# Optimization experiments

Measured on AMD Instinct MI355X. Metric: run time of the kernel, lower is better.

Reference implementation:

```python
import jax, jax.numpy as jnp
import numpy as np

MAX_LEN = 1024

def _lin(x, W, b=None):
    y = x @ W.T
    return y if b is None else y + b

def setup_inputs() -> dict:
    key = jax.random.key(0)
    ks = jax.random.split(key, 16)
    s = 0.05
    inp = {
        "x": jax.random.normal(ks[0], (8, 1024, 16), jnp.float32),
        "WQ": jax.random.normal(ks[1], (64, 16), jnp.float32) * s,
        "WK": jax.random.normal(ks[2], (64, 16), jnp.float32) * s,
        "VW1": jax.random.normal(ks[3], (16, 16), jnp.float32) * s,
        "Vb1": jnp.zeros((16,), jnp.float32),
        "VW2": jax.random.normal(ks[4], (16, 16), jnp.float32) * s,
        "Vb2": jnp.zeros((16,), jnp.float32),
        "VW3": jax.random.normal(ks[5], (8, 16), jnp.float32) * s,
        "Vb3": jnp.zeros((8,), jnp.float32),
        "PW1": jax.random.normal(ks[6], (64, 1), jnp.float32) * s,
        "Pb1": jnp.zeros((64,), jnp.float32),
        "PW2": jax.random.normal(ks[7], (64, 64), jnp.float32) * s,
        "Pb2": jnp.zeros((64,), jnp.float32),
        "PW3": jax.random.normal(ks[8], (64, 64), jnp.float32) * s,
        "Pb3": jnp.zeros((64,), jnp.float32),
        "PW4": jax.random.normal(ks[9], (32, 64), jnp.float32) * s,
        "Pb4": jnp.zeros((32,), jnp.float32),
        "offset": jnp.array([-10.0], jnp.float32),
        "HW1": jax.random.normal(ks[10], (256, 256), jnp.float32) * s,
        "Hb1": jnp.zeros((256,), jnp.float32),
        "HW2": jax.random.normal(ks[11], (256, 256), jnp.float32) * s,
        "Hb2": jnp.zeros((256,), jnp.float32),
        "HW3": jax.random.normal(ks[12], (4, 256), jnp.float32) * s,
        "Hb3": jnp.zeros((4,), jnp.float32),
    }
    return inp

def reference(x, WQ, WK, VW1, Vb1, VW2, Vb2, VW3, Vb3,
              PW1, Pb1, PW2, Pb2, PW3, Pb3, PW4, Pb4,
              offset, HW1, Hb1, HW2, Hb2, HW3, Hb3):
    B, L, _ = x.shape
    # Q/K projections and raw scores  [B, L, L]
    q = _lin(x, WQ)
    k = _lin(x, WK)
    a = jnp.einsum('bik,bjk->bij', q, k)
    d_k = q.shape[-1]
    # sigmoid attention with zeroed diagonal
    Iinf = 1.0 - jnp.eye(L, dtype=x.dtype)
    attention = jax.nn.sigmoid(a / jnp.sqrt(jnp.asarray(d_k, x.dtype)) + offset[0]) * Iinf
    # parametric set function: Phi MLP over t in [0,1]
    t = jnp.linspace(0.0, 1.0, MAX_LEN, dtype=x.dtype)[:L, None]  # [L, 1]
    h = jax.nn.relu(_lin(t, PW1, Pb1))
    h = jax.nn.relu(_lin(h, PW2, Pb2))
    h = jax.nn.relu(_lin(h, PW3, Pb3))
    SetPhi = _lin(h, PW4, Pb4)  # [L, set_dim]
    # relative-position gather: SetPhi[|i-j|] -> [L, L, set_dim]
    ar = jnp.arange(L)
    Tidx = jnp.abs(ar[:, None] - ar[None, :])
    rel = SetPhi[Tidx]
    set_values = jnp.einsum('bij,ijk->bik', attention, rel)  # [B, L, set_dim]
    # V MLP with sigmoid output  [B, L, vdim]
    v = jax.nn.relu(_lin(x, VW1, Vb1))
    v = jax.nn.relu(_lin(v, VW2, Vb2))
    v = jax.nn.sigmoid(_lin(v, VW3, Vb3))
    summarized = jnp.einsum('bij,bik->bjk', set_values, v)  # [B, set_dim, vdim]
    # head MLP + softmax (num_classes > 1)
    flat = summarized.reshape(B, -1)
    h = jax.nn.relu(_lin(flat, HW1, Hb1))
    h = jax.nn.relu(_lin(h, HW2, Hb2))
    return jax.nn.softmax(_lin(h, HW3, Hb3), axis=-1)
```

## Files before the change

kernel.cpp:

```cpp
#include <hip/hip_runtime.h>
#include <hip/hip_bf16.h>


#define LSEQ 1024
#define DK   64
#define EMB  16
#define VDIM 8

typedef __attribute__((ext_vector_type(8))) short bf16x8;
typedef __attribute__((ext_vector_type(4))) float f32x4;

__device__ __forceinline__ unsigned short f2bf(float f) {
  union { float f; unsigned u; } v; v.f = f;
  unsigned r = v.u + 0x7fffu + ((v.u >> 16) & 1u);
  return (unsigned short)(r >> 16);
}

__device__ __forceinline__ f32x4 mfma16(bf16x8 a, bf16x8 b, f32x4 c) {
  return __builtin_amdgcn_mfma_f32_16x16x32_bf16(a, b, c, 0, 0, 0);
}

__global__ __launch_bounds__(256) void prep_kernel(
    const float* __restrict__ x,  const float* __restrict__ WQ,  const float* __restrict__ WK,
    const float* __restrict__ VW1, const float* __restrict__ Vb1,
    const float* __restrict__ VW2, const float* __restrict__ Vb2,
    const float* __restrict__ VW3, const float* __restrict__ Vb3,
    const float* __restrict__ PW1, const float* __restrict__ Pb1,
    const float* __restrict__ PW2, const float* __restrict__ Pb2,
    const float* __restrict__ PW3, const float* __restrict__ Pb3,
    const float* __restrict__ PW4, const float* __restrict__ Pb4,
    unsigned short* __restrict__ qb, unsigned short* __restrict__ kb,
    unsigned short* __restrict__ phiT, float* __restrict__ vws,
    float* __restrict__ summar)
{
  __shared__ float s1[272];
  __shared__ float s2[272];
  int bid = blockIdx.x, tid = threadIdx.x;

  if (bid < 4096) {
    int g = bid * 256 + tid;
    int row = g >> 7, c = g & 127;
    const float* xr = x + row * EMB;
    const float* wr = ((c < 64) ? WQ : WK) + (c & 63) * EMB;
    float acc = 0.f;
    #pragma unroll
    for (int e = 0; e < 4; ++e) {
      f32x4 xv = *(const f32x4*)(xr + e * 4);
      f32x4 wv = *(const f32x4*)(wr + e * 4);
      acc += xv[0]*wv[0] + xv[1]*wv[1] + xv[2]*wv[2] + xv[3]*wv[3];
    }
    unsigned short* dst = (c < 64) ? qb : kb;
    dst[row * DK + (c & 63)] = f2bf(acc);

  } else if (bid < 4608) {
    int lb = bid - 4096;
    int r = tid >> 4, cc = tid & 15;
    int row = lb * 16 + r;
    const float* xr = x + row * EMB;
    float acc = Vb1[cc];
    #pragma unroll
    for (int e4 = 0; e4 < 4; ++e4) {
      f32x4 wv = *(const f32x4*)(VW1 + cc * 16 + e4 * 4);
      acc += xr[e4*4+0]*wv[0] + xr[e4*4+1]*wv[1] + xr[e4*4+2]*wv[2] + xr[e4*4+3]*wv[3];
    }
    s1[r * 17 + cc] = fmaxf(acc, 0.f);
    __syncthreads();
    acc = Vb2[cc];
    #pragma unroll
    for (int e4 = 0; e4 < 4; ++e4) {
      f32x4 wv = *(const f32x4*)(VW2 + cc * 16 + e4 * 4);
      acc += s1[r*17+e4*4+0]*wv[0] + s1[r*17+e4*4+1]*wv[1] + s1[r*17+e4*4+2]*wv[2] + s1[r*17+e4*4+3]*wv[3];
    }
    s2[r * 17 + cc] = fmaxf(acc, 0.f);
    __syncthreads();
    if (cc < 8) {
      acc = Vb3[cc];
      #pragma unroll
      for (int e4 = 0; e4 < 4; ++e4) {
        f32x4 wv = *(const f32x4*)(VW3 + cc * 16 + e4 * 4);
        acc += s2[r*17+e4*4+0]*wv[0] + s2[r*17+e4*4+1]*wv[1] + s2[r*17+e4*4+2]*wv[2] + s2[r*17+e4*4+3]*wv[3];
      }
      vws[row * VDIM + cc] = 1.f / (1.f + __expf(-acc));
    }

  } else if (bid < 4864) {
    int lb = bid - 4608;
    int r = tid >> 6, cc = tid & 63;
    int row = lb * 4 + r;
    float t = (float)row * (1.0f / 1023.0f);
    s1[r * 65 + cc] = fmaxf(PW1[cc] * t + Pb1[cc], 0.f);
    __syncthreads();
    float acc = Pb2[cc];
    #pragma unroll
    for (int e4 = 0; e4 < 16; ++e4) {
      f32x4 wv = *(const f32x4*)(PW2 + cc * 64 + e4 * 4);
      acc += s1[r*65+e4*4+0]*wv[0] + s1[r*65+e4*4+1]*wv[1] + s1[r*65+e4*4+2]*wv[2] + s1[r*65+e4*4+3]*wv[3];
    }
    s2[r * 65 + cc] = fmaxf(acc, 0.f);
    __syncthreads();
    acc = Pb3[cc];
    #pragma unroll
    for (int e4 = 0; e4 < 16; ++e4) {
      f32x4 wv = *(const f32x4*)(PW3 + cc * 64 + e4 * 4);
      acc += s2[r*65+e4*4+0]*wv[0] + s2[r*65+e4*4+1]*wv[1] + s2[r*65+e4*4+2]*wv[2] + s2[r*65+e4*4+3]*wv[3];
    }
    s1[r * 65 + cc] = fmaxf(acc, 0.f);
    __syncthreads();
    if (cc < 32) {
      acc = Pb4[cc];
      #pragma unroll
      for (int e4 = 0; e4 < 16; ++e4) {
        f32x4 wv = *(const f32x4*)(PW4 + cc * 64 + e4 * 4);
        acc += s1[r*65+e4*4+0]*wv[0] + s1[r*65+e4*4+1]*wv[1] + s1[r*65+e4*4+2]*wv[2] + s1[r*65+e4*4+3]*wv[3];
      }
      phiT[cc * LSEQ + row] = f2bf(acc);
    }

  } else {
    int idx = (bid - 4864) * 256 + tid;
    summar[idx] = 0.f;
  }
}

__global__ __launch_bounds__(512, 4) void attn_kernel(
    const unsigned short* __restrict__ qb, const unsigned short* __restrict__ kb,
    const unsigned short* __restrict__ phiT, const float* __restrict__ vws,
    const float* __restrict__ offs, float* __restrict__ summar)
{
  __shared__ float A2_s[16 * 1026];
  __shared__ float sv_w[8][16][17];
  __shared__ float v_s[16][8];

  int bid = blockIdx.x;
  int b  = bid >> 6;
  int i0 = (bid & 63) << 4;
  int tid = threadIdx.x;
  int lane = tid & 63, w = tid >> 6;
  int lr = lane & 15, lg = lane >> 4;

  for (int idx = tid; idx < 16 * 1026; idx += 512) A2_s[idx] = 0.f;
  if (tid < 128) v_s[tid >> 3][tid & 7] = vws[(b * LSEQ + i0 + (tid >> 3)) * VDIM + (tid & 7)];

  float off = offs[0];

  const unsigned short* qrow = qb + (size_t)(b * LSEQ + i0 + lr) * DK + lg * 8;
  bf16x8 afr0 = *(const bf16x8*)qrow;
  bf16x8 afr1 = *(const bf16x8*)(qrow + 32);

  const unsigned short* kbase = kb + (size_t)b * LSEQ * DK + (size_t)(w * 128 + lr) * DK + lg * 8;
  bf16x8 bk0[8], bk1[8];
  #pragma unroll
  for (int st = 0; st < 4; ++st) {
    bk0[2*st]   = *(const bf16x8*)(kbase + st * 16 * DK);
    bk0[2*st+1] = *(const bf16x8*)(kbase + st * 16 * DK + 32);
  }

  __syncthreads();

  #pragma unroll
  for (int st = 0; st < 4; ++st) {
    bk1[2*st]   = *(const bf16x8*)(kbase + (st + 4) * 16 * DK);
    bk1[2*st+1] = *(const bf16x8*)(kbase + (st + 4) * 16 * DK + 32);
  }

  #pragma unroll
  for (int st = 0; st < 4; ++st) {
    f32x4 acc = {0.f, 0.f, 0.f, 0.f};
    acc = mfma16(afr0, bk0[2*st], acc);
    acc = mfma16(afr1, bk0[2*st+1], acc);
    #pragma unroll
    for (int r2 = 0; r2 < 4; ++r2) {
      int row = 4 * lg + r2;
      int gi = i0 + row;
      int gj = w * 128 + st * 16 + lr;
      float s = (gi == gj) ? 0.f : 1.f / (1.f + __expf(-(acc[r2] * 0.125f + off)));
      int d = gi - gj; d = (d < 0) ? -d : d;
      unsafeAtomicAdd(&A2_s[row * 1026 + d], s);
    }
  }
  #pragma unroll
  for (int st = 0; st < 4; ++st) {
    f32x4 acc = {0.f, 0.f, 0.f, 0.f};
    acc = mfma16(afr0, bk1[2*st], acc);
    acc = mfma16(afr1, bk1[2*st+1], acc);
    #pragma unroll
    for (int r2 = 0; r2 < 4; ++r2) {
      int row = 4 * lg + r2;
      int gi = i0 + row;
      int gj = w * 128 + (st + 4) * 16 + lr;
      float s = (gi == gj) ? 0.f : 1.f / (1.f + __expf(-(acc[r2] * 0.125f + off)));
      int d = gi - gj; d = (d < 0) ? -d : d;
      unsafeAtomicAdd(&A2_s[row * 1026 + d], s);
    }
  }
  __syncthreads();

  {
    int ct = w & 1, kq = w >> 1;
    const unsigned short* ph = phiT + (ct * 16 + lr) * LSEQ + kq * 256 + lg * 8;
    bf16x8 pf[8];
    #pragma unroll
    for (int s = 0; s < 8; ++s) pf[s] = *(const bf16x8*)(ph + s * 32);
    const float* arow = A2_s + lr * 1026 + kq * 256 + lg * 8;
    f32x4 acc = {0.f, 0.f, 0.f, 0.f};
    #pragma unroll
    for (int s = 0; s < 8; ++s) {
      bf16x8 af;
      const float* ap = arow + s * 32;
      #pragma unroll
      for (int e = 0; e < 8; ++e) af[e] = (short)f2bf(ap[e]);
      acc = mfma16(af, pf[s], acc);
    }
    #pragma unroll
    for (int r2 = 0; r2 < 4; ++r2)
      sv_w[w][4 * lg + r2][lr] = acc[r2];
  }
  __syncthreads();

  if (tid < 256) {
    int sd = tid >> 3, kk = tid & 7;
    int ct = sd >> 4, cl = sd & 15;
    float a = 0.f;
    #pragma unroll
    for (int il = 0; il < 16; ++il) {
      float sv = sv_w[ct][il][cl] + sv_w[ct + 2][il][cl]
               + sv_w[ct + 4][il][cl] + sv_w[ct + 6][il][cl];
      a += sv * v_s[il][kk];
    }
    unsafeAtomicAdd(&summar[b * 256 + sd * 8 + kk], a);
  }
}

__global__ __launch_bounds__(1024) void head_kernel(
    const float* __restrict__ summar,
    const float* __restrict__ HW1, const float* __restrict__ Hb1,
    const float* __restrict__ HW2, const float* __restrict__ Hb2,
    const float* __restrict__ HW3, const float* __restrict__ Hb3,
    float* __restrict__ out)
{
  __shared__ float fb[256];
  __shared__ float part[4][260];
  __shared__ float lgt[4];
  int b = blockIdx.x, tid = threadIdx.x;
  int c = tid & 255, qt = tid >> 8;

  if (qt == 0) fb[c] = summar[b * 256 + c];
  __syncthreads();
  {
    const float* wr = HW1 + c * 256 + qt * 64;
    const float* xr = fb + qt * 64;
    float a = 0.f;
    #pragma unroll
    for (int e = 0; e < 16; ++e) {
      f32x4 wv = *(const f32x4*)(wr + e * 4);
      f32x4 xv = *(const f32x4*)(xr + e * 4);
      a += wv[0]*xv[0] + wv[1]*xv[1] + wv[2]*xv[2] + wv[3]*xv[3];
    }
    part[qt][c] = a;
  }
  __syncthreads();
  if (qt == 0)
    fb[c] = fmaxf(part[0][c] + part[1][c] + part[2][c] + part[3][c] + Hb1[c], 0.f);
  __syncthreads();
  {
    const float* wr = HW2 + c * 256 + qt * 64;
    const float* xr = fb + qt * 64;
    float a = 0.f;
    #pragma unroll
    for (int e = 0; e < 16; ++e) {
      f32x4 wv = *(const f32x4*)(wr + e * 4);
      f32x4 xv = *(const f32x4*)(xr + e * 4);
      a += wv[0]*xv[0] + wv[1]*xv[1] + wv[2]*xv[2] + wv[3]*xv[3];
    }
    part[qt][c] = a;
  }
  __syncthreads();
  if (qt == 0)
    fb[c] = fmaxf(part[0][c] + part[1][c] + part[2][c] + part[3][c] + Hb2[c], 0.f);
  __syncthreads();
  if (tid < 4) {
    float a = Hb3[tid];
    for (int e = 0; e < 256; ++e) a += fb[e] * HW3[tid * 256 + e];
    lgt[tid] = a;
  }
  __syncthreads();
  if (tid == 0) {
    float m = fmaxf(fmaxf(lgt[0], lgt[1]), fmaxf(lgt[2], lgt[3]));
    float e0 = __expf(lgt[0] - m), e1 = __expf(lgt[1] - m);
    float e2 = __expf(lgt[2] - m), e3 = __expf(lgt[3] - m);
    float s = e0 + e1 + e2 + e3;
    out[b * 4 + 0] = e0 / s;
    out[b * 4 + 1] = e1 / s;
    out[b * 4 + 2] = e2 / s;
    out[b * 4 + 3] = e3 / s;
  }
}

extern "C" void kernel_launch(void* const* d_in, const int* in_sizes, int n_in,
                              void* d_out, int out_size, void* d_ws, size_t ws_size,
                              hipStream_t stream)
{
  const float* x   = (const float*)d_in[0];
  const float* WQ  = (const float*)d_in[1];
  const float* WK  = (const float*)d_in[2];
  const float* VW1 = (const float*)d_in[3];
  const float* Vb1 = (const float*)d_in[4];
  const float* VW2 = (const float*)d_in[5];
  const float* Vb2 = (const float*)d_in[6];
  const float* VW3 = (const float*)d_in[7];
  const float* Vb3 = (const float*)d_in[8];
  const float* PW1 = (const float*)d_in[9];
  const float* Pb1 = (const float*)d_in[10];
  const float* PW2 = (const float*)d_in[11];
  const float* Pb2 = (const float*)d_in[12];
  const float* PW3 = (const float*)d_in[13];
  const float* Pb3 = (const float*)d_in[14];
  const float* PW4 = (const float*)d_in[15];
  const float* Pb4 = (const float*)d_in[16];
  const float* offs= (const float*)d_in[17];
  const float* HW1 = (const float*)d_in[18];
  const float* Hb1 = (const float*)d_in[19];
  const float* HW2 = (const float*)d_in[20];
  const float* Hb2 = (const float*)d_in[21];
  const float* HW3 = (const float*)d_in[22];
  const float* Hb3 = (const float*)d_in[23];

  char* ws = (char*)d_ws;
  unsigned short* qb   = (unsigned short*)(ws);
  unsigned short* kb   = (unsigned short*)(ws + (1u << 20));
  unsigned short* phiT = (unsigned short*)(ws + (2u << 20));
  float* vws    = (float*)(ws + (2u << 20) + (1u << 16));
  float* summar = (float*)(ws + (2u << 20) + (1u << 16) + (1u << 18));

  prep_kernel<<<dim3(4872), dim3(256), 0, stream>>>(
      x, WQ, WK, VW1, Vb1, VW2, Vb2, VW3, Vb3,
      PW1, Pb1, PW2, Pb2, PW3, Pb3, PW4, Pb4,
      qb, kb, phiT, vws, summar);

  attn_kernel<<<dim3(512), dim3(512), 0, stream>>>(
      qb, kb, phiT, vws, offs, summar);

  head_kernel<<<dim3(8), dim3(1024), 0, stream>>>(
      summar, HW1, Hb1, HW2, Hb2, HW3, Hb3, (float*)d_out);
}
```

Baseline: 189.0 us.

## Coarsen QK projection, hoist phi loads, and reduce V contraction with shuffles

The Q/K projection now has each thread compute 8 output channels for a row, cutting the prep grid from 4872 to 1288 blocks and reusing x loads. The attention kernel issues the phi fragment loads early so they overlap the zero-fill and score phase, and pads the shared A2 row stride. The final shared sv_w buffer, its barrier and the serial reduction are replaced by a per-wave multiply with V, cross-lane shuffle reduction and direct global atomics. The tradeoff is more global atomics per block and higher register pressure from holding the phi fragments live through the score phase.

```diff
diff --git a/kernel.cpp b/kernel.cpp
--- a/kernel.cpp
+++ b/kernel.cpp
@@ -6,6 +6,7 @@
 #define DK   64
 #define EMB  16
 #define VDIM 8
+#define A2S  1032
 
 typedef __attribute__((ext_vector_type(8))) short bf16x8;
 typedef __attribute__((ext_vector_type(4))) float f32x4;
@@ -37,23 +38,32 @@
   __shared__ float s2[272];
   int bid = blockIdx.x, tid = threadIdx.x;
 
-  if (bid < 4096) {
-    int g = bid * 256 + tid;
-    int row = g >> 7, c = g & 127;
+  if (bid < 512) {
+    int row = bid * 16 + (tid >> 4);
+    int c0 = (tid & 15) * 8;
     const float* xr = x + row * EMB;
-    const float* wr = ((c < 64) ? WQ : WK) + (c & 63) * EMB;
-    float acc = 0.f;
-    #pragma unroll
-    for (int e = 0; e < 4; ++e) {
-      f32x4 xv = *(const f32x4*)(xr + e * 4);
-      f32x4 wv = *(const f32x4*)(wr + e * 4);
-      acc += xv[0]*wv[0] + xv[1]*wv[1] + xv[2]*wv[2] + xv[3]*wv[3];
-    }
-    unsigned short* dst = (c < 64) ? qb : kb;
-    dst[row * DK + (c & 63)] = f2bf(acc);
-
-  } else if (bid < 4608) {
-    int lb = bid - 4096;
+    f32x4 xv0 = *(const f32x4*)(xr);
+    f32x4 xv1 = *(const f32x4*)(xr + 4);
+    f32x4 xv2 = *(const f32x4*)(xr + 8);
+    f32x4 xv3 = *(const f32x4*)(xr + 12);
+    #pragma unroll
+    for (int u = 0; u < 8; ++u) {
+      int c = c0 + u;
+      const float* wr = ((c < 64) ? WQ : WK) + (c & 63) * EMB;
+      f32x4 wv0 = *(const f32x4*)(wr);
+      f32x4 wv1 = *(const f32x4*)(wr + 4);
+      f32x4 wv2 = *(const f32x4*)(wr + 8);
+      f32x4 wv3 = *(const f32x4*)(wr + 12);
+      float acc = xv0[0]*wv0[0]+xv0[1]*wv0[1]+xv0[2]*wv0[2]+xv0[3]*wv0[3]
+                + xv1[0]*wv1[0]+xv1[1]*wv1[1]+xv1[2]*wv1[2]+xv1[3]*wv1[3]
+                + xv2[0]*wv2[0]+xv2[1]*wv2[1]+xv2[2]*wv2[2]+xv2[3]*wv2[3]
+                + xv3[0]*wv3[0]+xv3[1]*wv3[1]+xv3[2]*wv3[2]+xv3[3]*wv3[3];
+      unsigned short* dst = (c < 64) ? qb : kb;
+      dst[row * DK + (c & 63)] = f2bf(acc);
+    }
+
+  } else if (bid < 1024) {
+    int lb = bid - 512;
     int r = tid >> 4, cc = tid & 15;
     int row = lb * 16 + r;
     const float* xr = x + row * EMB;
@@ -83,8 +93,8 @@
       vws[row * VDIM + cc] = 1.f / (1.f + __expf(-acc));
     }
 
-  } else if (bid < 4864) {
-    int lb = bid - 4608;
+  } else if (bid < 1280) {
+    int lb = bid - 1024;
     int r = tid >> 6, cc = tid & 63;
     int row = lb * 4 + r;
     float t = (float)row * (1.0f / 1023.0f);
@@ -117,7 +127,7 @@
     }
 
   } else {
-    int idx = (bid - 4864) * 256 + tid;
+    int idx = (bid - 1280) * 256 + tid;
     summar[idx] = 0.f;
   }
 }
@@ -127,8 +137,7 @@
     const unsigned short* __restrict__ phiT, const float* __restrict__ vws,
     const float* __restrict__ offs, float* __restrict__ summar)
 {
-  __shared__ float A2_s[16 * 1026];
-  __shared__ float sv_w[8][16][17];
+  __shared__ float A2_s[16 * A2S];
   __shared__ float v_s[16][8];
 
   int bid = blockIdx.x;
@@ -138,25 +147,31 @@
   int lane = tid & 63, w = tid >> 6;
   int lr = lane & 15, lg = lane >> 4;
 
-  for (int idx = tid; idx < 16 * 1026; idx += 512) A2_s[idx] = 0.f;
-  if (tid < 128) v_s[tid >> 3][tid & 7] = vws[(b * LSEQ + i0 + (tid >> 3)) * VDIM + (tid & 7)];
-
-  float off = offs[0];
-
   const unsigned short* qrow = qb + (size_t)(b * LSEQ + i0 + lr) * DK + lg * 8;
   bf16x8 afr0 = *(const bf16x8*)qrow;
   bf16x8 afr1 = *(const bf16x8*)(qrow + 32);
 
+  int ct = w & 1, kq = w >> 1;
+  const unsigned short* ph = phiT + (ct * 16 + lr) * LSEQ + kq * 256 + lg * 8;
+  bf16x8 pf[8];
+  #pragma unroll
+  for (int s = 0; s < 8; ++s) pf[s] = *(const bf16x8*)(ph + s * 32);
+
   const unsigned short* kbase = kb + (size_t)b * LSEQ * DK + (size_t)(w * 128 + lr) * DK + lg * 8;
-  bf16x8 bk0[8], bk1[8];
+  bf16x8 bk0[8];
   #pragma unroll
   for (int st = 0; st < 4; ++st) {
     bk0[2*st]   = *(const bf16x8*)(kbase + st * 16 * DK);
     bk0[2*st+1] = *(const bf16x8*)(kbase + st * 16 * DK + 32);
   }
 
-  __syncthreads();
-
+  float off = offs[0];
+  if (tid < 128) v_s[tid >> 3][tid & 7] = vws[(b * LSEQ + i0 + (tid >> 3)) * VDIM + (tid & 7)];
+
+  for (int idx = tid; idx < 16 * A2S; idx += 512) A2_s[idx] = 0.f;
+  __syncthreads();
+
+  bf16x8 bk1[8];
   #pragma unroll
   for (int st = 0; st < 4; ++st) {
     bk1[2*st]   = *(const bf16x8*)(kbase + (st + 4) * 16 * DK);
@@ -175,7 +190,7 @@
       int gj = w * 128 + st * 16 + lr;
       float s = (gi == gj) ? 0.f : 1.f / (1.f + __expf(-(acc[r2] * 0.125f + off)));
       int d = gi - gj; d = (d < 0) ? -d : d;
-      unsafeAtomicAdd(&A2_s[row * 1026 + d], s);
+      unsafeAtomicAdd(&A2_s[row * A2S + d], s);
     }
   }
   #pragma unroll
@@ -190,19 +205,14 @@
       int gj = w * 128 + (st + 4) * 16 + lr;
       float s = (gi == gj) ? 0.f : 1.f / (1.f + __expf(-(acc[r2] * 0.125f + off)));
       int d = gi - gj; d = (d < 0) ? -d : d;
-      unsafeAtomicAdd(&A2_s[row * 1026 + d], s);
-    }
-  }
-  __syncthreads();
-
+      unsafeAtomicAdd(&A2_s[row * A2S + d], s);
+    }
+  }
+  __syncthreads();
+
+  f32x4 acc = {0.f, 0.f, 0.f, 0.f};
   {
-    int ct = w & 1, kq = w >> 1;
-    const unsigned short* ph = phiT + (ct * 16 + lr) * LSEQ + kq * 256 + lg * 8;
-    bf16x8 pf[8];
-    #pragma unroll
-    for (int s = 0; s < 8; ++s) pf[s] = *(const bf16x8*)(ph + s * 32);
-    const float* arow = A2_s + lr * 1026 + kq * 256 + lg * 8;
-    f32x4 acc = {0.f, 0.f, 0.f, 0.f};
+    const float* arow = A2_s + lr * A2S + kq * 256 + lg * 8;
     #pragma unroll
     for (int s = 0; s < 8; ++s) {
       bf16x8 af;
@@ -211,23 +221,33 @@
       for (int e = 0; e < 8; ++e) af[e] = (short)f2bf(ap[e]);
       acc = mfma16(af, pf[s], acc);
     }
-    #pragma unroll
-    for (int r2 = 0; r2 < 4; ++r2)
-      sv_w[w][4 * lg + r2][lr] = acc[r2];
-  }
-  __syncthreads();
-
-  if (tid < 256) {
-    int sd = tid >> 3, kk = tid & 7;
-    int ct = sd >> 4, cl = sd & 15;
-    float a = 0.f;
-    #pragma unroll
-    for (int il = 0; il < 16; ++il) {
-      float sv = sv_w[ct][il][cl] + sv_w[ct + 2][il][cl]
-               + sv_w[ct + 4][il][cl] + sv_w[ct + 6][il][cl];
-      a += sv * v_s[il][kk];
-    }
-    unsafeAtomicAdd(&summar[b * 256 + sd * 8 + kk], a);
+  }
+
+  {
+    float p[8];
+    #pragma unroll
+    for (int kk = 0; kk < 8; ++kk) p[kk] = 0.f;
+    #pragma unroll
+    for (int r2 = 0; r2 < 4; ++r2) {
+      int row = 4 * lg + r2;
+      f32x4 va = *(const f32x4*)&v_s[row][0];
+      f32x4 vb = *(const f32x4*)&v_s[row][4];
+      p[0] += acc[r2] * va[0];  p[1] += acc[r2] * va[1];
+      p[2] += acc[r2] * va[2];  p[3] += acc[r2] * va[3];
+      p[4] += acc[r2] * vb[0];  p[5] += acc[r2] * vb[1];
+      p[6] += acc[r2] * vb[2];  p[7] += acc[r2] * vb[3];
+    }
+    #pragma unroll
+    for (int kk = 0; kk < 8; ++kk) {
+      p[kk] += __shfl_xor(p[kk], 16);
+      p[kk] += __shfl_xor(p[kk], 32);
+    }
+    if (lg == 0) {
+      float* dst = summar + b * 256 + (ct * 16 + lr) * 8;
+      #pragma unroll
+      for (int kk = 0; kk < 8; ++kk)
+        unsafeAtomicAdd(&dst[kk], p[kk]);
+    }
   }
 }
 
@@ -332,7 +352,7 @@
   float* vws    = (float*)(ws + (2u << 20) + (1u << 16));
   float* summar = (float*)(ws + (2u << 20) + (1u << 16) + (1u << 18));
 
-  prep_kernel<<<dim3(4872), dim3(256), 0, stream>>>(
+  prep_kernel<<<dim3(1288), dim3(256), 0, stream>>>(
       x, WQ, WK, VW1, Vb1, VW2, Vb2, VW3, Vb3,
       PW1, Pb1, PW2, Pb2, PW3, Pb3, PW4, Pb4,
       qb, kb, phiT, vws, summar);
```

Result: slower. 256.4 us (+35.7%).
